# Performance work log

Measured on AMD Instinct MI355X. Metric: run time of the kernel, lower is better.

The kernel has to match this reference:

```python
import jax, jax.numpy as jnp
import numpy as np

TEMPERATURE = 0.1
TOP_K = 5


def setup_inputs() -> dict:
    key = jax.random.key(0)
    k1, k2 = jax.random.split(key)
    latent = jax.random.normal(k1, (128, 8, 250, 16), dtype=jnp.float32)
    codebook = jax.random.normal(k2, (1024, 8, 250, 16), dtype=jnp.float32) * 0.5
    usage_count = jnp.zeros((1024,), dtype=jnp.float32)
    return {"latent": latent, "codebook": codebook, "usage_count": usage_count}


def reference(latent, codebook, usage_count):
    # soft_quantize_latent
    B = latent.shape[0]
    C = codebook.shape[0]
    lf = latent.reshape(B, -1).astype(jnp.float32)            # [B, D]
    cf = codebook.reshape(C, -1).astype(jnp.float32)          # [C, D]
    # cdist p=2 via expanded squared norms (single GEMM)
    d2 = (jnp.sum(lf * lf, axis=1, keepdims=True)
          + jnp.sum(cf * cf, axis=1)[None, :]
          - 2.0 * (lf @ cf.T))                                 # [B, C]
    dist = jnp.sqrt(jnp.maximum(d2, 0.0))
    # top-k smallest distances
    neg_top, top_idx = jax.lax.top_k(-dist, TOP_K)             # [B, K]
    top_dist = -neg_top
    weights = jax.nn.softmax(-top_dist / TEMPERATURE, axis=1)  # [B, K]
    # weighted codebook combination (gather K rows per batch element)
    quantized = jnp.einsum('bk,bkd->bd', weights, cf[top_idx]).reshape(latent.shape)
    quantized = quantized.astype(latent.dtype)
    # usage update is no_grad in torch: scatter-add stopped weights
    usage_new = usage_count.at[top_idx.reshape(-1)].add(
        jax.lax.stop_gradient(weights).reshape(-1))
    main_indices = top_idx[:, 0]
    main_distances = top_dist[:, 0]
    return (quantized, main_indices, main_distances, usage_new)
```

## Files before the change

kernel.cpp:

```cpp
#include <hip/hip_runtime.h>
#include <math.h>

#define M_B   128
#define N_C   1024
#define K_D   32000
#define NTILE 64
#define KCHUNK 320
#define KSTEP 64
#define NSTAGE (KCHUNK / KSTEP)
#define LDSK  (KSTEP + 8)
#define TOPK  5
#define TEMP  0.1f

typedef short bf16x8 __attribute__((ext_vector_type(8)));
typedef float f32x4  __attribute__((ext_vector_type(4)));

#define WS_CROSS  0
#define WS_CNORM  131072
#define WS_LNORM  132096
#define WS_TOPI   132224
#define WS_TOPW   132864
#define WS_ZERO_N 132224

__global__ void prep(float* __restrict__ ws, const float* __restrict__ usage_in,
                     float* __restrict__ usage_out) {
  const int i = blockIdx.x * 256 + threadIdx.x;
  if (i < WS_ZERO_N) ws[i] = 0.f;
  if (i < N_C) usage_out[i] = usage_in[i];
}

__device__ inline void cvt8(const float4 p0, const float4 p1, uint4& hi,
                            uint4& lo) {
  const unsigned int u0 = __float_as_uint(p0.x), u1 = __float_as_uint(p0.y);
  const unsigned int u2 = __float_as_uint(p0.z), u3 = __float_as_uint(p0.w);
  const unsigned int u4 = __float_as_uint(p1.x), u5 = __float_as_uint(p1.y);
  const unsigned int u6 = __float_as_uint(p1.z), u7 = __float_as_uint(p1.w);
  hi.x = (u0 >> 16) | (u1 & 0xFFFF0000u);
  hi.y = (u2 >> 16) | (u3 & 0xFFFF0000u);
  hi.z = (u4 >> 16) | (u5 & 0xFFFF0000u);
  hi.w = (u6 >> 16) | (u7 & 0xFFFF0000u);
  const float l0 = p0.x - __uint_as_float(u0 & 0xFFFF0000u);
  const float l1 = p0.y - __uint_as_float(u1 & 0xFFFF0000u);
  const float l2 = p0.z - __uint_as_float(u2 & 0xFFFF0000u);
  const float l3 = p0.w - __uint_as_float(u3 & 0xFFFF0000u);
  const float l4 = p1.x - __uint_as_float(u4 & 0xFFFF0000u);
  const float l5 = p1.y - __uint_as_float(u5 & 0xFFFF0000u);
  const float l6 = p1.z - __uint_as_float(u6 & 0xFFFF0000u);
  const float l7 = p1.w - __uint_as_float(u7 & 0xFFFF0000u);
  lo.x = (__float_as_uint(l0) >> 16) | (__float_as_uint(l1) & 0xFFFF0000u);
  lo.y = (__float_as_uint(l2) >> 16) | (__float_as_uint(l3) & 0xFFFF0000u);
  lo.z = (__float_as_uint(l4) >> 16) | (__float_as_uint(l5) & 0xFFFF0000u);
  lo.w = (__float_as_uint(l6) >> 16) | (__float_as_uint(l7) & 0xFFFF0000u);
}

__device__ inline float sq8(const float4 p0, const float4 p1) {
  return p0.x * p0.x + p0.y * p0.y + p0.z * p0.z + p0.w * p0.w +
         p1.x * p1.x + p1.y * p1.y + p1.z * p1.z + p1.w * p1.w;
}

__global__ __launch_bounds__(256, 4) void gemm_dist(
    const float* __restrict__ latent, const float* __restrict__ codebook,
    float* __restrict__ cross, float* __restrict__ cnorm,
    float* __restrict__ lnorm) {
  __shared__ alignas(16) unsigned short Bh[2][NTILE][LDSK];
  __shared__ alignas(16) unsigned short Bl[2][NTILE][LDSK];

  const int tid  = threadIdx.x;
  const int nt   = blockIdx.x;
  const int kc   = blockIdx.y;
  const int wave = tid >> 6;
  const int lane = tid & 63;
  const int lrow = lane & 15;
  const int quad = lane >> 4;

  const int brow = tid >> 2;
  const int bcol = (tid & 3) * 16;

  f32x4 acc[2][4];
#pragma unroll
  for (int mt = 0; mt < 2; ++mt)
#pragma unroll
    for (int n = 0; n < 4; ++n) {
      acc[mt][n][0] = 0.f; acc[mt][n][1] = 0.f;
      acc[mt][n][2] = 0.f; acc[mt][n][3] = 0.f;
    }
  float lsq[2] = {0.f, 0.f};
  float csq = 0.f;

  const int kbase = kc * KCHUNK;
  const float* browp = codebook + (size_t)(nt * NTILE + brow) * K_D;

#pragma unroll
  for (int u = 0; u < 2; ++u) {
    const int kk = kbase + bcol + u * 8;
    const float4 p0 = *reinterpret_cast<const float4*>(browp + kk);
    const float4 p1 = *reinterpret_cast<const float4*>(browp + kk + 4);
    uint4 hi, lo;
    cvt8(p0, p1, hi, lo);
    *reinterpret_cast<uint4*>(&Bh[0][brow][bcol + u * 8]) = hi;
    *reinterpret_cast<uint4*>(&Bl[0][brow][bcol + u * 8]) = lo;
    csq += sq8(p0, p1);
  }

  int cur = 0;
  for (int s = 0; s < NSTAGE; ++s) {
    const int k0 = kbase + s * KSTEP;
    float4 ap[2][2][2];
#pragma unroll
    for (int kh = 0; kh < 2; ++kh)
#pragma unroll
      for (int mt = 0; mt < 2; ++mt) {
        const float* ar = latent +
                          (size_t)(wave * 32 + mt * 16 + lrow) * K_D + k0 +
                          kh * 32 + quad * 8;
        ap[kh][mt][0] = *reinterpret_cast<const float4*>(ar);
        ap[kh][mt][1] = *reinterpret_cast<const float4*>(ar + 4);
      }
    float4 bp[2][2];
    if (s + 1 < NSTAGE) {
      const int kn = kbase + (s + 1) * KSTEP + bcol;
#pragma unroll
      for (int u = 0; u < 2; ++u) {
        bp[u][0] = *reinterpret_cast<const float4*>(browp + kn + u * 8);
        bp[u][1] = *reinterpret_cast<const float4*>(browp + kn + u * 8 + 4);
      }
    }
    __syncthreads();
#pragma unroll
    for (int kh = 0; kh < 2; ++kh) {
      bf16x8 ah[2], al[2];
#pragma unroll
      for (int mt = 0; mt < 2; ++mt) {
        uint4 hi, lo;
        cvt8(ap[kh][mt][0], ap[kh][mt][1], hi, lo);
        ah[mt] = *reinterpret_cast<bf16x8*>(&hi);
        al[mt] = *reinterpret_cast<bf16x8*>(&lo);
        if (nt == 0) lsq[mt] += sq8(ap[kh][mt][0], ap[kh][mt][1]);
      }
      const int kf = kh * 32 + quad * 8;
#pragma unroll
      for (int n = 0; n < 4; ++n) {
        const bf16x8 bh =
            *reinterpret_cast<const bf16x8*>(&Bh[cur][n * 16 + lrow][kf]);
        const bf16x8 bl =
            *reinterpret_cast<const bf16x8*>(&Bl[cur][n * 16 + lrow][kf]);
#pragma unroll
        for (int mt = 0; mt < 2; ++mt) {
          acc[mt][n] = __builtin_amdgcn_mfma_f32_16x16x32_bf16(
              ah[mt], bh, acc[mt][n], 0, 0, 0);
          acc[mt][n] = __builtin_amdgcn_mfma_f32_16x16x32_bf16(
              ah[mt], bl, acc[mt][n], 0, 0, 0);
          acc[mt][n] = __builtin_amdgcn_mfma_f32_16x16x32_bf16(
              al[mt], bh, acc[mt][n], 0, 0, 0);
        }
      }
    }
    if (s + 1 < NSTAGE) {
      const int nxt = cur ^ 1;
#pragma unroll
      for (int u = 0; u < 2; ++u) {
        uint4 hi, lo;
        cvt8(bp[u][0], bp[u][1], hi, lo);
        *reinterpret_cast<uint4*>(&Bh[nxt][brow][bcol + u * 8]) = hi;
        *reinterpret_cast<uint4*>(&Bl[nxt][brow][bcol + u * 8]) = lo;
        csq += sq8(bp[u][0], bp[u][1]);
      }
    }
    cur ^= 1;
  }

#pragma unroll
  for (int mt = 0; mt < 2; ++mt) {
    const int mrow0 = wave * 32 + mt * 16 + quad * 4;
#pragma unroll
    for (int n = 0; n < 4; ++n) {
      const int col = nt * NTILE + n * 16 + lrow;
#pragma unroll
      for (int r = 0; r < 4; ++r)
        atomicAdd(cross + (size_t)(mrow0 + r) * N_C + col, acc[mt][n][r]);
    }
  }

  csq += __shfl_down(csq, 2, 4);
  csq += __shfl_down(csq, 1, 4);
  if ((tid & 3) == 0) atomicAdd(cnorm + nt * NTILE + brow, csq);
  if (nt == 0) {
#pragma unroll
    for (int mt = 0; mt < 2; ++mt) {
      lsq[mt] += __shfl_down(lsq[mt], 32);
      lsq[mt] += __shfl_down(lsq[mt], 16);
      if (lane < 16) atomicAdd(lnorm + wave * 32 + mt * 16 + lane, lsq[mt]);
    }
  }
}

__global__ __launch_bounds__(256) void finalize(
    const float* __restrict__ cross, const float* __restrict__ cnorm,
    const float* __restrict__ lnorm, float* __restrict__ out_idx,
    float* __restrict__ out_dist, float* __restrict__ out_usage,
    int* __restrict__ topidx, float* __restrict__ topw) {
  const int b = blockIdx.x;
  const int tid = threadIdx.x;
  __shared__ float rv[256];
  __shared__ int ri[256];
  __shared__ float seld[TOPK];
  __shared__ int selj[TOPK];

  float d[4];
  bool used[4];
  const float ln = lnorm[b];
#pragma unroll
  for (int i = 0; i < 4; i++) {
    const int j = i * 256 + tid;
    d[i] = ln + cnorm[j] - 2.f * cross[b * N_C + j];
    used[i] = false;
  }
  for (int it = 0; it < TOPK; ++it) {
    float best = 3.4e38f;
    int bj = N_C;
#pragma unroll
    for (int i = 0; i < 4; i++) {
      const int j = i * 256 + tid;
      if (!used[i] && d[i] < best) { best = d[i]; bj = j; }
    }
    rv[tid] = best;
    ri[tid] = bj;
    __syncthreads();
    for (int off = 128; off > 0; off >>= 1) {
      if (tid < off) {
        const float ov = rv[tid + off];
        const int oj = ri[tid + off];
        if (ov < rv[tid] || (ov == rv[tid] && oj < ri[tid])) {
          rv[tid] = ov;
          ri[tid] = oj;
        }
      }
      __syncthreads();
    }
    const int jw = ri[0];
    const float dw = rv[0];
    if (tid == 0) { selj[it] = jw; seld[it] = dw; }
    if ((jw & 255) == tid) used[jw >> 8] = true;
    __syncthreads();
  }
  if (tid == 0) {
    float dist[TOPK], w[TOPK], wsum = 0.f;
#pragma unroll
    for (int k = 0; k < TOPK; k++) dist[k] = sqrtf(fmaxf(seld[k], 0.f));
#pragma unroll
    for (int k = 0; k < TOPK; k++) {
      w[k] = expf((dist[0] - dist[k]) / TEMP);
      wsum += w[k];
    }
#pragma unroll
    for (int k = 0; k < TOPK; k++) {
      w[k] /= wsum;
      topidx[b * TOPK + k] = selj[k];
      topw[b * TOPK + k] = w[k];
      atomicAdd(out_usage + selj[k], w[k]);
    }
    out_idx[b] = (float)selj[0];
    out_dist[b] = dist[0];
  }
}

__global__ __launch_bounds__(256) void quantize(
    const float* __restrict__ codebook, const int* __restrict__ topidx,
    const float* __restrict__ topw, float* __restrict__ out) {
  const int b = blockIdx.y;
  const int dc = blockIdx.x;
  const int tid = threadIdx.x;
  int idx[TOPK];
  float w[TOPK];
#pragma unroll
  for (int k = 0; k < TOPK; k++) {
    idx[k] = topidx[b * TOPK + k];
    w[k] = topw[b * TOPK + k];
  }
  const int f4base = dc * 1000;
#pragma unroll
  for (int s = 0; s < 4; s++) {
    const int f = tid + s * 256;
    if (f < 1000) {
      const int dpos = (f4base + f) * 4;
      float4 q = {0.f, 0.f, 0.f, 0.f};
#pragma unroll
      for (int k = 0; k < TOPK; k++) {
        const float4 c = *reinterpret_cast<const float4*>(
            codebook + (size_t)idx[k] * K_D + dpos);
        q.x += w[k] * c.x;
        q.y += w[k] * c.y;
        q.z += w[k] * c.z;
        q.w += w[k] * c.w;
      }
      *reinterpret_cast<float4*>(out + (size_t)b * K_D + dpos) = q;
    }
  }
}

extern "C" void kernel_launch(void* const* d_in, const int* in_sizes, int n_in,
                              void* d_out, int out_size, void* d_ws,
                              size_t ws_size, hipStream_t stream) {
  const float* latent = (const float*)d_in[0];
  const float* codebook = (const float*)d_in[1];
  const float* usage_in = (const float*)d_in[2];

  float* out = (float*)d_out;
  float* quant = out;
  float* out_idx = out + 4096000;
  float* out_dist = out + 4096128;
  float* out_usage = out + 4096256;

  float* ws = (float*)d_ws;
  float* cross = ws + WS_CROSS;
  float* cnorm = ws + WS_CNORM;
  float* lnorm = ws + WS_LNORM;
  int* topidx = (int*)(ws + WS_TOPI);
  float* topw = ws + WS_TOPW;

  prep<<<(WS_ZERO_N + 255) / 256, 256, 0, stream>>>(ws, usage_in, out_usage);
  gemm_dist<<<dim3(16, 100), 256, 0, stream>>>(latent, codebook, cross, cnorm,
                                               lnorm);
  finalize<<<128, 256, 0, stream>>>(cross, cnorm, lnorm, out_idx, out_dist,
                                    out_usage, topidx, topw);
  quantize<<<dim3(8, 128), 256, 0, stream>>>(codebook, topidx, topw, quant);
}
```

Baseline: 256.5 us.

## Pre-split latent into bf16 hi/lo planes and deepen codebook prefetch

A new prep kernel converts the latent once into bf16 hi/lo planes, stored in the output buffer as scratch, and computes per-row partial norms there. The GEMM then loads ready bf16 fragments instead of re-converting fp32 latent in each of the 16 column tiles. The change also doubles KCHUNK, which halves the split-K grid and the atomics, and prefetches codebook two stages ahead. The trade-off is an extra pass over the latent, more registers under launch bounds of 3, and fewer blocks to fill the GPU.

Measured after the change: 277.0 us. 1.08x slower.

```diff
diff --git a/kernel.cpp b/kernel.cpp
--- a/kernel.cpp
+++ b/kernel.cpp
@@ -5,7 +5,7 @@
 #define N_C   1024
 #define K_D   32000
 #define NTILE 64
-#define KCHUNK 320
+#define KCHUNK 640
 #define KSTEP 64
 #define NSTAGE (KCHUNK / KSTEP)
 #define LDSK  (KSTEP + 8)
@@ -15,19 +15,12 @@
 typedef short bf16x8 __attribute__((ext_vector_type(8)));
 typedef float f32x4  __attribute__((ext_vector_type(4)));
 
-#define WS_CROSS  0
-#define WS_CNORM  131072
-#define WS_LNORM  132096
-#define WS_TOPI   132224
-#define WS_TOPW   132864
-#define WS_ZERO_N 132224
-
-__global__ void prep(float* __restrict__ ws, const float* __restrict__ usage_in,
-                     float* __restrict__ usage_out) {
-  const int i = blockIdx.x * 256 + threadIdx.x;
-  if (i < WS_ZERO_N) ws[i] = 0.f;
-  if (i < N_C) usage_out[i] = usage_in[i];
-}
+#define WS_CROSS   0
+#define WS_CNORM   131072
+#define WS_ZERO_N  132096
+#define WS_TOPI    132224
+#define WS_TOPW    132864
+#define WS_LNORM16 133504
 
 __device__ inline void cvt8(const float4 p0, const float4 p1, uint4& hi,
                             uint4& lo) {
@@ -58,10 +51,55 @@
          p1.x * p1.x + p1.y * p1.y + p1.z * p1.z + p1.w * p1.w;
 }
 
-__global__ __launch_bounds__(256, 4) void gemm_dist(
-    const float* __restrict__ latent, const float* __restrict__ codebook,
-    float* __restrict__ cross, float* __restrict__ cnorm,
-    float* __restrict__ lnorm) {
+__global__ __launch_bounds__(256) void prep(
+    const float* __restrict__ latent, const float* __restrict__ usage_in,
+    float* __restrict__ ws, float* __restrict__ usage_out,
+    unsigned short* __restrict__ aplanes) {
+  const int tid = threadIdx.x;
+  const int bx = blockIdx.x;
+  const int by = blockIdx.y;
+  if (bx == 16) {
+    const int id2 = by * 256 + tid;
+#pragma unroll
+    for (int j = 0; j < 5; ++j) {
+      const int idx = id2 + j * 32768;
+      if (idx < WS_ZERO_N) ws[idx] = 0.f;
+    }
+    if (id2 < N_C) usage_out[id2] = usage_in[id2];
+    return;
+  }
+  const int u = bx * 256 + tid;
+  float lsq = 0.f;
+  if (u < 4000) {
+    const int k = u * 8;
+    const float* src = latent + (size_t)by * K_D + k;
+    const float4 p0 = *reinterpret_cast<const float4*>(src);
+    const float4 p1 = *reinterpret_cast<const float4*>(src + 4);
+    uint4 hi, lo;
+    cvt8(p0, p1, hi, lo);
+    unsigned short* ah = aplanes + (size_t)by * K_D + k;
+    *reinterpret_cast<uint4*>(ah) = hi;
+    *reinterpret_cast<uint4*>(ah + (size_t)M_B * K_D) = lo;
+    lsq = sq8(p0, p1);
+  }
+  lsq += __shfl_down(lsq, 32);
+  lsq += __shfl_down(lsq, 16);
+  lsq += __shfl_down(lsq, 8);
+  lsq += __shfl_down(lsq, 4);
+  lsq += __shfl_down(lsq, 2);
+  lsq += __shfl_down(lsq, 1);
+  __shared__ float wpart[4];
+  if ((tid & 63) == 0) wpart[tid >> 6] = lsq;
+  __syncthreads();
+  if (tid == 0)
+    (ws + WS_LNORM16)[by * 16 + bx] =
+        wpart[0] + wpart[1] + wpart[2] + wpart[3];
+}
+
+__global__ __launch_bounds__(256, 3) void gemm_dist(
+    const unsigned short* __restrict__ aplanes,
+    const float* __restrict__ codebook, float* __restrict__ cross,
+    float* __restrict__ cnorm) {
   __shared__ alignas(16) unsigned short Bh[2][NTILE][LDSK];
   __shared__ alignas(16) unsigned short Bl[2][NTILE][LDSK];
 
@@ -84,11 +122,11 @@
       acc[mt][n][0] = 0.f; acc[mt][n][1] = 0.f;
       acc[mt][n][2] = 0.f; acc[mt][n][3] = 0.f;
     }
-  float lsq[2] = {0.f, 0.f};
   float csq = 0.f;
 
   const int kbase = kc * KCHUNK;
   const float* browp = codebook + (size_t)(nt * NTILE + brow) * K_D;
+  const unsigned short* al_base = aplanes + (size_t)M_B * K_D;
 
 #pragma unroll
   for (int u = 0; u < 2; ++u) {
@@ -101,42 +139,44 @@
     *reinterpret_cast<uint4*>(&Bl[0][brow][bcol + u * 8]) = lo;
     csq += sq8(p0, p1);
   }
+  float4 bp[2][2];
+  {
+    const int kn = kbase + KSTEP + bcol;
+#pragma unroll
+    for (int u = 0; u < 2; ++u) {
+      bp[u][0] = *reinterpret_cast<const float4*>(browp + kn + u * 8);
+      bp[u][1] = *reinterpret_cast<const float4*>(browp + kn + u * 8 + 4);
+    }
+  }
 
   int cur = 0;
   for (int s = 0; s < NSTAGE; ++s) {
+    __syncthreads();
     const int k0 = kbase + s * KSTEP;
-    float4 ap[2][2][2];
-#pragma unroll
-    for (int kh = 0; kh < 2; ++kh)
-#pragma unroll
-      for (int mt = 0; mt < 2; ++mt) {
-        const float* ar = latent +
-                          (size_t)(wave * 32 + mt * 16 + lrow) * K_D + k0 +
-                          kh * 32 + quad * 8;
-        ap[kh][mt][0] = *reinterpret_cast<const float4*>(ar);
-        ap[kh][mt][1] = *reinterpret_cast<const float4*>(ar + 4);
-      }
-    float4 bp[2][2];
-    if (s + 1 < NSTAGE) {
-      const int kn = kbase + (s + 1) * KSTEP + bcol;
+    bf16x8 ah[2][2], al[2][2];
+#pragma unroll
+    for (int mt = 0; mt < 2; ++mt) {
+      const size_t ro =
+          (size_t)(wave * 32 + mt * 16 + lrow) * K_D + k0 + quad * 8;
+#pragma unroll
+      for (int kh = 0; kh < 2; ++kh) {
+        ah[mt][kh] =
+            *reinterpret_cast<const bf16x8*>(aplanes + ro + kh * 32);
+        al[mt][kh] =
+            *reinterpret_cast<const bf16x8*>(al_base + ro + kh * 32);
+      }
+    }
+    float4 bq[2][2];
+    if (s + 2 < NSTAGE) {
+      const int kn = kbase + (s + 2) * KSTEP + bcol;
 #pragma unroll
       for (int u = 0; u < 2; ++u) {
-        bp[u][0] = *reinterpret_cast<const float4*>(browp + kn + u * 8);
-        bp[u][1] = *reinterpret_cast<const float4*>(browp + kn + u * 8 + 4);
-      }
-    }
-    __syncthreads();
+        bq[u][0] = *reinterpret_cast<const float4*>(browp + kn + u * 8);
+        bq[u][1] = *reinterpret_cast<const float4*>(browp + kn + u * 8 + 4);
+      }
+    }
 #pragma unroll
     for (int kh = 0; kh < 2; ++kh) {
-      bf16x8 ah[2], al[2];
-#pragma unroll
-      for (int mt = 0; mt < 2; ++mt) {
-        uint4 hi, lo;
-        cvt8(ap[kh][mt][0], ap[kh][mt][1], hi, lo);
-        ah[mt] = *reinterpret_cast<bf16x8*>(&hi);
-        al[mt] = *reinterpret_cast<bf16x8*>(&lo);
-        if (nt == 0) lsq[mt] += sq8(ap[kh][mt][0], ap[kh][mt][1]);
-      }
       const int kf = kh * 32 + quad * 8;
 #pragma unroll
       for (int n = 0; n < 4; ++n) {
@@ -147,11 +187,11 @@
 #pragma unroll
         for (int mt = 0; mt < 2; ++mt) {
           acc[mt][n] = __builtin_amdgcn_mfma_f32_16x16x32_bf16(
-              ah[mt], bh, acc[mt][n], 0, 0, 0);
+              ah[mt][kh], bh, acc[mt][n], 0, 0, 0);
           acc[mt][n] = __builtin_amdgcn_mfma_f32_16x16x32_bf16(
-              ah[mt], bl, acc[mt][n], 0, 0, 0);
+              ah[mt][kh], bl, acc[mt][n], 0, 0, 0);
           acc[mt][n] = __builtin_amdgcn_mfma_f32_16x16x32_bf16(
-              al[mt], bh, acc[mt][n], 0, 0, 0);
+              al[mt][kh], bh, acc[mt][n], 0, 0, 0);
         }
       }
     }
@@ -166,6 +206,13 @@
         csq += sq8(bp[u][0], bp[u][1]);
       }
     }
+    if (s + 2 < NSTAGE) {
+#pragma unroll
+      for (int u = 0; u < 2; ++u) {
+        bp[u][0] = bq[u][0];
+        bp[u][1] = bq[u][1];
+      }
+    }
     cur ^= 1;
   }
 
@@ -184,19 +231,11 @@
   csq += __shfl_down(csq, 2, 4);
   csq += __shfl_down(csq, 1, 4);
   if ((tid & 3) == 0) atomicAdd(cnorm + nt * NTILE + brow, csq);
-  if (nt == 0) {
-#pragma unroll
-    for (int mt = 0; mt < 2; ++mt) {
-      lsq[mt] += __shfl_down(lsq[mt], 32);
-      lsq[mt] += __shfl_down(lsq[mt], 16);
-      if (lane < 16) atomicAdd(lnorm + wave * 32 + mt * 16 + lane, lsq[mt]);
-    }
-  }
 }
 
 __global__ __launch_bounds__(256) void finalize(
     const float* __restrict__ cross, const float* __restrict__ cnorm,
-    const float* __restrict__ lnorm, float* __restrict__ out_idx,
+    const float* __restrict__ lnorm16, float* __restrict__ out_idx,
     float* __restrict__ out_dist, float* __restrict__ out_usage,
     int* __restrict__ topidx, float* __restrict__ topw) {
   const int b = blockIdx.x;
@@ -206,9 +245,12 @@
   __shared__ float seld[TOPK];
   __shared__ int selj[TOPK];
 
+  float ln = 0.f;
+#pragma unroll
+  for (int x = 0; x < 16; ++x) ln += lnorm16[b * 16 + x];
+
   float d[4];
   bool used[4];
-  const float ln = lnorm[b];
 #pragma unroll
   for (int i = 0; i < 4; i++) {
     const int j = i * 256 + tid;
@@ -314,14 +356,16 @@
   float* ws = (float*)d_ws;
   float* cross = ws + WS_CROSS;
   float* cnorm = ws + WS_CNORM;
-  float* lnorm = ws + WS_LNORM;
+  float* lnorm16 = ws + WS_LNORM16;
   int* topidx = (int*)(ws + WS_TOPI);
   float* topw = ws + WS_TOPW;
 
-  prep<<<(WS_ZERO_N + 255) / 256, 256, 0, stream>>>(ws, usage_in, out_usage);
-  gemm_dist<<<dim3(16, 100), 256, 0, stream>>>(latent, codebook, cross, cnorm,
-                                               lnorm);
-  finalize<<<128, 256, 0, stream>>>(cross, cnorm, lnorm, out_idx, out_dist,
+  unsigned short* aplanes = (unsigned short*)quant;
+
+  prep<<<dim3(17, 128), 256, 0, stream>>>(latent, usage_in, ws, out_usage,
+                                          aplanes);
+  gemm_dist<<<dim3(16, 50), 256, 0, stream>>>(aplanes, codebook, cross, cnorm);
+  finalize<<<128, 256, 0, stream>>>(cross, cnorm, lnorm16, out_idx, out_dist,
                                     out_usage, topidx, topw);
   quantize<<<dim3(8, 128), 256, 0, stream>>>(codebook, topidx, topw, quant);
 }
```

## Single-buffer LDS B tile with explicit barriers and raise occupancy target

Applied to the files above, without the earlier changes.

Replaces the double-buffered LDS codebook tile with a single buffer guarded by two lightweight barriers per stage (waitcnt on lgkm plus s_barrier and a scheduling fence). This halves the LDS footprint and raises the launch_bounds occupancy hint from 4 to 6 blocks per CU. The stage loop is also fully unrolled. The trade-off is an extra barrier per stage, which serialises LDS writes against MFMA reads and may cost latency hiding. The higher occupancy target may also force register spills.

Measured after the change: 455.5 us. 77.6% more time.

```diff
diff --git a/kernel.cpp b/kernel.cpp
--- a/kernel.cpp
+++ b/kernel.cpp
@@ -21,6 +21,13 @@
 #define WS_TOPI   132224
 #define WS_TOPW   132864
 #define WS_ZERO_N 132224
+
+#define LDS_BARRIER()                                        \
+  do {                                                       \
+    asm volatile("s_waitcnt lgkmcnt(0)" ::: "memory");       \
+    __builtin_amdgcn_s_barrier();                            \
+    __builtin_amdgcn_sched_barrier(0);                       \
+  } while (0)
 
 __global__ void prep(float* __restrict__ ws, const float* __restrict__ usage_in,
                      float* __restrict__ usage_out) {
@@ -58,12 +65,12 @@
          p1.x * p1.x + p1.y * p1.y + p1.z * p1.z + p1.w * p1.w;
 }
 
-__global__ __launch_bounds__(256, 4) void gemm_dist(
+__global__ __launch_bounds__(256, 6) void gemm_dist(
     const float* __restrict__ latent, const float* __restrict__ codebook,
     float* __restrict__ cross, float* __restrict__ cnorm,
     float* __restrict__ lnorm) {
-  __shared__ alignas(16) unsigned short Bh[2][NTILE][LDSK];
-  __shared__ alignas(16) unsigned short Bl[2][NTILE][LDSK];
+  __shared__ alignas(16) unsigned short Bh[NTILE][LDSK];
+  __shared__ alignas(16) unsigned short Bl[NTILE][LDSK];
 
   const int tid  = threadIdx.x;
   const int nt   = blockIdx.x;
@@ -97,12 +104,13 @@
     const float4 p1 = *reinterpret_cast<const float4*>(browp + kk + 4);
     uint4 hi, lo;
     cvt8(p0, p1, hi, lo);
-    *reinterpret_cast<uint4*>(&Bh[0][brow][bcol + u * 8]) = hi;
-    *reinterpret_cast<uint4*>(&Bl[0][brow][bcol + u * 8]) = lo;
+    *reinterpret_cast<uint4*>(&Bh[brow][bcol + u * 8]) = hi;
+    *reinterpret_cast<uint4*>(&Bl[brow][bcol + u * 8]) = lo;
     csq += sq8(p0, p1);
   }
-
-  int cur = 0;
+  LDS_BARRIER();
+
+#pragma unroll
   for (int s = 0; s < NSTAGE; ++s) {
     const int k0 = kbase + s * KSTEP;
     float4 ap[2][2][2];
@@ -116,16 +124,15 @@
         ap[kh][mt][0] = *reinterpret_cast<const float4*>(ar);
         ap[kh][mt][1] = *reinterpret_cast<const float4*>(ar + 4);
       }
-    float4 bp[2][2];
+    float4 bq[2][2];
     if (s + 1 < NSTAGE) {
       const int kn = kbase + (s + 1) * KSTEP + bcol;
 #pragma unroll
       for (int u = 0; u < 2; ++u) {
-        bp[u][0] = *reinterpret_cast<const float4*>(browp + kn + u * 8);
-        bp[u][1] = *reinterpret_cast<const float4*>(browp + kn + u * 8 + 4);
-      }
-    }
-    __syncthreads();
+        bq[u][0] = *reinterpret_cast<const float4*>(browp + kn + u * 8);
+        bq[u][1] = *reinterpret_cast<const float4*>(browp + kn + u * 8 + 4);
+      }
+    }
 #pragma unroll
     for (int kh = 0; kh < 2; ++kh) {
       bf16x8 ah[2], al[2];
@@ -141,9 +148,9 @@
 #pragma unroll
       for (int n = 0; n < 4; ++n) {
         const bf16x8 bh =
-            *reinterpret_cast<const bf16x8*>(&Bh[cur][n * 16 + lrow][kf]);
+            *reinterpret_cast<const bf16x8*>(&Bh[n * 16 + lrow][kf]);
         const bf16x8 bl =
-            *reinterpret_cast<const bf16x8*>(&Bl[cur][n * 16 + lrow][kf]);
+            *reinterpret_cast<const bf16x8*>(&Bl[n * 16 + lrow][kf]);
 #pragma unroll
         for (int mt = 0; mt < 2; ++mt) {
           acc[mt][n] = __builtin_amdgcn_mfma_f32_16x16x32_bf16(
@@ -156,17 +163,17 @@
       }
     }
     if (s + 1 < NSTAGE) {
-      const int nxt = cur ^ 1;
+      LDS_BARRIER();
 #pragma unroll
       for (int u = 0; u < 2; ++u) {
         uint4 hi, lo;
-        cvt8(bp[u][0], bp[u][1], hi, lo);
-        *reinterpret_cast<uint4*>(&Bh[nxt][brow][bcol + u * 8]) = hi;
-        *reinterpret_cast<uint4*>(&Bl[nxt][brow][bcol + u * 8]) = lo;
-        csq += sq8(bp[u][0], bp[u][1]);
-      }
-    }
-    cur ^= 1;
+        cvt8(bq[u][0], bq[u][1], hi, lo);
+        *reinterpret_cast<uint4*>(&Bh[brow][bcol + u * 8]) = hi;
+        *reinterpret_cast<uint4*>(&Bl[brow][bcol + u * 8]) = lo;
+        csq += sq8(bq[u][0], bq[u][1]);
+      }
+      LDS_BARRIER();
+    }
   }
 
 #pragma unroll
```
